# Kernel tuning notes

Measured on AMD Instinct MI355X. Metric: run time of the kernel, lower is better.

Reference implementation:

```python
import jax, jax.numpy as jnp
import numpy as np

C = 256
NUM_HEADS = 8
HEAD_DIM = C // NUM_HEADS
SCALE = HEAD_DIM ** -0.5


def setup_inputs() -> dict:
    key = jax.random.key(0)
    ks = jax.random.split(key, 10)
    B, H, W = 2, 64, 64
    s = 0.02
    return {
        "spatial_feat": jax.random.normal(ks[0], (B, C, H, W), jnp.float32),
        "freq_feat": jax.random.normal(ks[1], (B, C, H, W), jnp.float32),
        "wq": jax.random.normal(ks[2], (C, C), jnp.float32) * s,
        "bq": jax.random.normal(ks[3], (C,), jnp.float32) * s,
        "wk": jax.random.normal(ks[4], (C, C), jnp.float32) * s,
        "bk": jax.random.normal(ks[5], (C,), jnp.float32) * s,
        "wv": jax.random.normal(ks[6], (C, C), jnp.float32) * s,
        "bv": jax.random.normal(ks[7], (C,), jnp.float32) * s,
        "wo": jax.random.normal(ks[8], (C, C), jnp.float32) * s,
        "bo": jax.random.normal(ks[9], (C,), jnp.float32) * s,
    }


def _proj(x, w, b):
    # 1x1 conv == channel-mixing matmul: (O,C) x (B,C,H,W) -> (B,O,H,W)
    return jnp.einsum('oc,bchw->bohw', w, x) + b[None, :, None, None]


def _heads(x, B, HW):
    return x.reshape(B, NUM_HEADS, HEAD_DIM, HW)


def _cross_attend(q_src, kv_src, wq, bq, wk, bk, wv, bv, wo, bo):
    B, Cc, H, W = q_src.shape
    HW = H * W
    q = _heads(_proj(q_src, wq, bq), B, HW)   # (B, h, d, N)
    k = _heads(_proj(kv_src, wk, bk), B, HW)
    v = _heads(_proj(kv_src, wv, bv), B, HW)
    # attn[b,h,m,n] = q[...,m] . k[...,n]
    attn = jnp.einsum('bhdm,bhdn->bhmn', q, k) * SCALE
    attn = jax.nn.softmax(attn, axis=-1)
    # out[...,m] = sum_n v[...,n] * attn[m,n]
    out = jnp.einsum('bhdn,bhmn->bhdm', v, attn)
    out = out.reshape(B, Cc, H, W)
    return _proj(out, wo, bo)


def reference(spatial_feat, freq_feat, wq, bq, wk, bk, wv, bv, wo, bo):
    spatial_attended = spatial_feat + _cross_attend(
        spatial_feat, freq_feat, wq, bq, wk, bk, wv, bv, wo, bo)
    freq_attended = freq_feat + _cross_attend(
        freq_feat, spatial_feat, wq, bq, wk, bk, wv, bv, wo, bo)
    return spatial_attended + freq_attended
```

## Files before the change

kernel.cpp:

```cpp
#include <hip/hip_runtime.h>
#include <hip/hip_bf16.h>

#define B_ 2
#define C_ 256
#define NH_ 8
#define D_ 32
#define N_ 4096
#define SCALE_ 0.17677669529663689f
#define QSC_ 0.25505277f

typedef __hip_bfloat16 bf16;
typedef __attribute__((ext_vector_type(8))) short sx8;
typedef __attribute__((ext_vector_type(4))) short sx4;
typedef __attribute__((ext_vector_type(4))) float fx4;
typedef __attribute__((ext_vector_type(4))) int ix4;

__device__ __forceinline__ float b2f(bf16 x) { return __bfloat162float(x); }
__device__ __forceinline__ bf16 f2b(float x) { return __float2bfloat16(x); }
__device__ __forceinline__ short fbs(float x) { bf16 h = __float2bfloat16(x); return *(short*)&h; }
__device__ __forceinline__ float sbf(short s) { bf16 h = *(bf16*)&s; return __bfloat162float(h); }

#if __has_builtin(__builtin_amdgcn_exp2f)
__device__ __forceinline__ float fexp2(float x) { return __builtin_amdgcn_exp2f(x); }
#else
__device__ __forceinline__ float fexp2(float x) { return exp2f(x); }
#endif

__device__ __forceinline__ unsigned pkbf_tr(float x, float y) {
#if __has_builtin(__builtin_amdgcn_perm)
  return __builtin_amdgcn_perm(__builtin_bit_cast(unsigned, y),
                               __builtin_bit_cast(unsigned, x), 0x07060302u);
#else
  unsigned a = __builtin_bit_cast(unsigned, x) >> 16;
  unsigned b = __builtin_bit_cast(unsigned, y) & 0xFFFF0000u;
  return a | b;
#endif
}
__device__ __forceinline__ void pl32swap(unsigned &a, unsigned &b) {
  asm volatile("v_permlane32_swap_b32 %0, %1" : "+v"(a), "+v"(b));
}
__device__ __forceinline__ void pl16swap(unsigned &a, unsigned &b) {
  asm volatile("v_permlane16_swap_b32 %0, %1" : "+v"(a), "+v"(b));
}

__global__ __launch_bounds__(256)
void convert_kernel(const float* __restrict__ spatial,
                    const float* __restrict__ freq,
                    const float* __restrict__ wq, const float* __restrict__ wk,
                    const float* __restrict__ wv, const float* __restrict__ wo,
                    bf16* __restrict__ xb, bf16* __restrict__ wb,
                    bf16* __restrict__ wob) {
  const int tid = threadIdx.x;
  if (blockIdx.z == 4) {
    int base = (blockIdx.y * 64 + blockIdx.x) * 256 + tid;
    #pragma unroll
    for (int i = 0; i < 4; ++i) {
      int idx = base + i * 65536;
      if (idx < 196608) {
        const float* src = (idx < 65536) ? wq : (idx < 131072) ? wk : wv;
        wb[idx] = f2b(src[idx & 65535]);
      } else {
        wob[idx - 196608] = f2b(wo[idx - 196608]);
      }
    }
    return;
  }

  const int p0 = blockIdx.x * 64;
  const int c0 = blockIdx.y * 64;
  const int z  = blockIdx.z;
  const int s = z >> 1, b = z & 1;
  const float* x = (s == 0) ? spatial : freq;

  __shared__ float ls[64][65];

  const int pp = tid & 63, cb = tid >> 6;
  #pragma unroll
  for (int i = 0; i < 16; ++i) {
    int c = cb + 4 * i;
    ls[c][pp] = x[(size_t)(b * C_ + c0 + c) * N_ + p0 + pp];
  }
  __syncthreads();

  #pragma unroll
  for (int i = 0; i < 2; ++i) {
    int j = tid + 256 * i;
    int p = j >> 3, ck = (j & 7) * 8;
    short tmp[8];
    #pragma unroll
    for (int u = 0; u < 8; ++u) tmp[u] = fbs(ls[ck + u][p]);
    *(sx8*)(xb + ((size_t)z * N_ + p0 + p) * C_ + c0 + ck) = *(sx8*)tmp;
  }
}

__global__ __launch_bounds__(256)
void qkv_gemm_kernel(const bf16* __restrict__ wb, const bf16* __restrict__ xb,
                     const float* __restrict__ bq, const float* __restrict__ bk,
                     const float* __restrict__ bv,
                     bf16* __restrict__ qhf, bf16* __restrict__ khf,
                     bf16* __restrict__ vhf) {
  const int tid = threadIdx.x;
  const int p0 = blockIdx.x * 128;
  const int o0 = blockIdx.y * 128;
  const int z  = blockIdx.z;

  const int lane = tid & 63, w = tid >> 6;
  const int ml = lane & 15, Q4 = (lane >> 4) * 4, Q8 = (lane >> 4) * 8;
  const int ow = (w >> 1) * 64, pw = (w & 1) * 64;

  __shared__ __align__(16) short asb[128 * 72];
  __shared__ __align__(16) short bsb[128 * 72];
  __shared__ float bias_s[128];

  if (tid < 128) {
    int o = o0 + tid;
    bias_s[tid] = (o < 256) ? bq[o] : (o < 512) ? bk[o - 256] : bv[o - 512];
  }

  const fx4 z4 = {0.f, 0.f, 0.f, 0.f};
  fx4 acc[4][4];
  #pragma unroll
  for (int ot = 0; ot < 4; ++ot)
    #pragma unroll
    for (int pt = 0; pt < 4; ++pt) acc[ot][pt] = z4;

  const int sr = tid >> 1, scu = (tid & 1) * 32;
  for (int k0 = 0; k0 < 256; k0 += 64) {
    __syncthreads();
    #pragma unroll
    for (int u = 0; u < 4; ++u) {
      *(sx8*)&asb[sr * 72 + scu + u * 8] =
          *(const sx8*)&wb[(o0 + sr) * 256 + k0 + scu + u * 8];
      *(sx8*)&bsb[sr * 72 + scu + u * 8] =
          *(const sx8*)(xb + ((size_t)z * N_ + p0 + sr) * C_ + k0 + scu + u * 8);
    }
    __syncthreads();
    #pragma unroll
    for (int kk = 0; kk < 2; ++kk) {
      sx8 af[4], bfr[4];
      #pragma unroll
      for (int t = 0; t < 4; ++t)
        af[t] = *(sx8*)&asb[(ow + t * 16 + ml) * 72 + kk * 32 + Q8];
      #pragma unroll
      for (int t = 0; t < 4; ++t)
        bfr[t] = *(sx8*)&bsb[(pw + t * 16 + ml) * 72 + kk * 32 + Q8];
      #pragma unroll
      for (int ot = 0; ot < 4; ++ot)
        #pragma unroll
        for (int pt = 0; pt < 4; ++pt)
          acc[ot][pt] = __builtin_amdgcn_mfma_f32_16x16x32_bf16(
              af[ot], bfr[pt], acc[ot][pt], 0, 0, 0);
    }
  }

  if (o0 < 512) {
    bf16* dst = (o0 < 256) ? qhf : khf;
    const int ob = (o0 < 256) ? o0 : o0 - 256;
    const float scl = (o0 < 256) ? QSC_ : 1.f;
    #pragma unroll
    for (int ot = 0; ot < 4; ++ot) {
      const int og = ob + ow + ot * 16 + Q4;
      #pragma unroll
      for (int pt = 0; pt < 4; ++pt) {
        int p = p0 + pw + pt * 16 + ml;
        short tmp[4];
        #pragma unroll
        for (int r = 0; r < 4; ++r)
          tmp[r] = fbs((acc[ot][pt][r] + bias_s[ow + ot * 16 + Q4 + r]) * scl);
        *(sx4*)(dst + (((size_t)z * NH_ + (og >> 5)) * N_ + p) * D_ + (og & 31)) =
            *(sx4*)tmp;
      }
    }
  } else {
    #pragma unroll
    for (int ot = 0; ot < 4; ++ot)
      #pragma unroll
      for (int pt = 0; pt < 4; ++pt) {
        int p = p0 + pw + pt * 16 + ml;
        #pragma unroll
        for (int r = 0; r < 4; ++r) {
          int lo = ow + ot * 16 + Q4 + r;
          int rho = (o0 - 512) + lo;
          int h = rho >> 5, d = rho & 31;
          size_t basev = ((size_t)z * NH_ + h) * D_ * N_;
          vhf[basev + (size_t)(((p >> 5) * 2) + (d >> 4)) * 512 +
              (d & 15) * 32 + (p & 31)] = f2b(acc[ot][pt][r] + bias_s[lo]);
        }
      }
  }
}

__device__ __forceinline__ void attn_tile(const sx8 kf[4], const sx8 vf[2][2],
                                          const sx8 qf[4], sx8 onesf,
                                          fx4 acc[4][2], fx4 lacc[4]) {
  const fx4 z4 = {0.f, 0.f, 0.f, 0.f};
  #pragma unroll
  for (int s4 = 0; s4 < 4; ++s4) {
    fx4 st[4];
    __builtin_amdgcn_s_setprio(1);
    #pragma unroll
    for (int t = 0; t < 4; ++t)
      st[t] = __builtin_amdgcn_mfma_f32_16x16x32_bf16(kf[t], qf[s4], z4, 0, 0, 0);
    __builtin_amdgcn_s_setprio(0);

    unsigned T[4][2];
    #pragma unroll
    for (int t = 0; t < 4; ++t) {
      float e0 = fexp2(st[t][0]), e1 = fexp2(st[t][1]);
      float e2 = fexp2(st[t][2]), e3 = fexp2(st[t][3]);
      T[t][0] = pkbf_tr(e0, e1);
      T[t][1] = pkbf_tr(e2, e3);
    }
    pl32swap(T[0][0], T[1][0]); pl16swap(T[0][0], T[1][0]);
    pl32swap(T[0][1], T[1][1]); pl16swap(T[0][1], T[1][1]);
    pl32swap(T[2][0], T[3][0]); pl16swap(T[2][0], T[3][0]);
    pl32swap(T[2][1], T[3][1]); pl16swap(T[2][1], T[3][1]);
    ix4 p0 = {(int)T[0][0], (int)T[0][1], (int)T[1][0], (int)T[1][1]};
    ix4 p1 = {(int)T[2][0], (int)T[2][1], (int)T[3][0], (int)T[3][1]};
    sx8 pf0 = *(sx8*)&p0;
    sx8 pf1 = *(sx8*)&p1;

    __builtin_amdgcn_s_setprio(1);
    lacc[s4] = __builtin_amdgcn_mfma_f32_16x16x32_bf16(onesf, pf0, lacc[s4], 0, 0, 0);
    lacc[s4] = __builtin_amdgcn_mfma_f32_16x16x32_bf16(onesf, pf1, lacc[s4], 0, 0, 0);
    #pragma unroll
    for (int dt = 0; dt < 2; ++dt) {
      fx4 a = acc[s4][dt];
      a = __builtin_amdgcn_mfma_f32_16x16x32_bf16(vf[dt][0], pf0, a, 0, 0, 0);
      a = __builtin_amdgcn_mfma_f32_16x16x32_bf16(vf[dt][1], pf1, a, 0, 0, 0);
      acc[s4][dt] = a;
    }
    __builtin_amdgcn_s_setprio(0);
  }
}

__global__ __launch_bounds__(256, 2)
void attn_kernel(const bf16* __restrict__ qhf, const bf16* __restrict__ khf,
                 const bf16* __restrict__ vhf, bf16* __restrict__ attoT) {
  const int tid  = threadIdx.x;
  const int m0   = blockIdx.x * 256;
  const int h    = blockIdx.y;
  const int z    = blockIdx.z;
  const int s = z >> 1, b = z & 1;
  const int zo = ((1 - s) << 1) | b;

  const bf16* qz = qhf + ((size_t)z  * NH_ + h) * N_ * D_;
  const bf16* kz = khf + ((size_t)zo * NH_ + h) * N_ * D_;
  const bf16* vz = vhf + ((size_t)zo * NH_ + h) * D_ * N_;

  const int lane = tid & 63;
  const int w    = tid >> 6;
  const int ml   = lane & 15;
  const int q4   = lane >> 4;
  const int Q4   = q4 * 4;
  const int Q8   = q4 * 8;

  sx8 qf[4];
  #pragma unroll
  for (int s4 = 0; s4 < 4; ++s4)
    qf[s4] = *(const sx8*)(qz + (size_t)(m0 + w * 64 + s4 * 16 + ml) * D_ + Q8);

  sx8 onesf;
  #pragma unroll
  for (int u = 0; u < 8; ++u) onesf[u] = (short)0x3F80;

  const fx4 z4 = {0.f, 0.f, 0.f, 0.f};
  fx4 acc[4][2];
  #pragma unroll
  for (int s4 = 0; s4 < 4; ++s4) { acc[s4][0] = z4; acc[s4][1] = z4; }
  fx4 lacc[4] = {z4, z4, z4, z4};

  const bf16* kbase = kz + (size_t)ml * D_ + Q8;
  const bf16* vbase = vz + (size_t)ml * 32 + Q8;

#define LDK(n0, kf)                                                          \
  {                                                                          \
    _Pragma("unroll") for (int t = 0; t < 4; ++t)                            \
        kf[t] = *(const sx8*)(kbase + (size_t)((n0) + t * 16) * D_);         \
  }
#define LDV(n0, vf)                                                          \
  {                                                                          \
    _Pragma("unroll") for (int dt = 0; dt < 2; ++dt)                         \
        _Pragma("unroll") for (int c = 0; c < 2; ++c)                        \
            vf[dt][c] = *(const sx8*)(vbase +                                \
                (size_t)(((n0) >> 5) + c) * 1024 + dt * 512);                \
  }

  sx8 kfA[4], kfB[4], vfA[2][2], vfB[2][2];
  LDK(0, kfA);
  LDV(0, vfA);

  #pragma unroll 1
  for (int n0 = 0; n0 < N_; n0 += 128) {
    const int nn = n0 + 64;
    LDK(nn, kfB);
    LDV(nn, vfB);
    attn_tile(kfA, vfA, qf, onesf, acc, lacc);

    const int nn2 = (nn + 64 < N_) ? nn + 64 : 0;
    LDK(nn2, kfA);
    LDV(nn2, vfA);
    attn_tile(kfB, vfB, qf, onesf, acc, lacc);
  }
#undef LDK
#undef LDV

  #pragma unroll
  for (int s4 = 0; s4 < 4; ++s4) {
    float inv = 1.f / lacc[s4][0];
    int col = m0 + w * 64 + s4 * 16 + ml;
    #pragma unroll
    for (int dt = 0; dt < 2; ++dt) {
      short tmp[4];
      #pragma unroll
      for (int r = 0; r < 4; ++r) tmp[r] = fbs(acc[s4][dt][r] * inv);
      *(sx4*)(attoT + ((size_t)z * N_ + col) * C_ + h * D_ + dt * 16 + Q4) =
          *(sx4*)tmp;
    }
  }
}

__global__ __launch_bounds__(256)
void out_proj_kernel(const bf16* __restrict__ wob, const bf16* __restrict__ attoT,
                     const float* __restrict__ spatial,
                     const float* __restrict__ freq,
                     const float* __restrict__ bo, float* __restrict__ out) {
  const int tid = threadIdx.x;
  const int p0 = blockIdx.x * 64;
  const int o0 = blockIdx.y * 64;
  const int b  = blockIdx.z;

  const int lane = tid & 63, w = tid >> 6;
  const int ml = lane & 15, Q4 = (lane >> 4) * 4, Q8 = (lane >> 4) * 8;
  const int ow = (w >> 1) * 32, pw = (w & 1) * 32;

  __shared__ __align__(16) short asb[64 * 72];
  __shared__ __align__(16) short bsb[64 * 72];
  __shared__ float bo_s[64];

  if (tid < 64) bo_s[tid] = 2.f * bo[o0 + tid];

  const bf16* at0 = attoT + (size_t)(0 + b) * N_ * C_;
  const bf16* at1 = attoT + (size_t)(2 + b) * N_ * C_;

  const fx4 z4 = {0.f, 0.f, 0.f, 0.f};
  fx4 acc[2][2];
  #pragma unroll
  for (int ot = 0; ot < 2; ++ot)
    #pragma unroll
    for (int pt = 0; pt < 2; ++pt) acc[ot][pt] = z4;

  for (int k0 = 0; k0 < 256; k0 += 64) {
    __syncthreads();
    #pragma unroll
    for (int i = 0; i < 2; ++i) {
      int j = tid + 256 * i;
      int r = j >> 3, cu = (j & 7) * 8;
      *(sx8*)&asb[r * 72 + cu] = *(const sx8*)&wob[(o0 + r) * 256 + k0 + cu];
      sx8 va = *(const sx8*)(at0 + (size_t)(p0 + r) * C_ + k0 + cu);
      sx8 vb2 = *(const sx8*)(at1 + (size_t)(p0 + r) * C_ + k0 + cu);
      short tmp[8];
      #pragma unroll
      for (int u = 0; u < 8; ++u) tmp[u] = fbs(sbf(va[u]) + sbf(vb2[u]));
      *(sx8*)&bsb[r * 72 + cu] = *(sx8*)tmp;
    }
    __syncthreads();
    #pragma unroll
    for (int kk = 0; kk < 2; ++kk) {
      sx8 af[2], bfr[2];
      #pragma unroll
      for (int t = 0; t < 2; ++t)
        af[t] = *(sx8*)&asb[(ow + t * 16 + ml) * 72 + kk * 32 + Q8];
      #pragma unroll
      for (int t = 0; t < 2; ++t)
        bfr[t] = *(sx8*)&bsb[(pw + t * 16 + ml) * 72 + kk * 32 + Q8];
      #pragma unroll
      for (int ot = 0; ot < 2; ++ot)
        #pragma unroll
        for (int pt = 0; pt < 2; ++pt)
          acc[ot][pt] = __builtin_amdgcn_mfma_f32_16x16x32_bf16(
              af[ot], bfr[pt], acc[ot][pt], 0, 0, 0);
    }
  }

  #pragma unroll
  for (int ot = 0; ot < 2; ++ot)
    #pragma unroll
    for (int pt = 0; pt < 2; ++pt) {
      int p = p0 + pw + pt * 16 + ml;
      #pragma unroll
      for (int r = 0; r < 4; ++r) {
        int ol = ow + ot * 16 + Q4 + r;
        size_t off = ((size_t)b * C_ + o0 + ol) * N_ + p;
        out[off] = acc[ot][pt][r] + bo_s[ol] + spatial[off] + freq[off];
      }
    }
}

extern "C" void kernel_launch(void* const* d_in, const int* in_sizes, int n_in,
                              void* d_out, int out_size, void* d_ws, size_t ws_size,
                              hipStream_t stream) {
  const float* spatial = (const float*)d_in[0];
  const float* freq    = (const float*)d_in[1];
  const float* wq = (const float*)d_in[2];
  const float* bq = (const float*)d_in[3];
  const float* wk = (const float*)d_in[4];
  const float* bk = (const float*)d_in[5];
  const float* wv = (const float*)d_in[6];
  const float* bv = (const float*)d_in[7];
  const float* wo = (const float*)d_in[8];
  const float* bo = (const float*)d_in[9];
  float* out = (float*)d_out;

  const size_t SZ = (size_t)2 * B_ * N_ * C_;
  bf16* xb    = (bf16*)d_ws;
  bf16* qhf   = xb + SZ;
  bf16* khf   = qhf + SZ;
  bf16* vhf   = khf + SZ;
  bf16* attoT = vhf + SZ;
  bf16* wb    = attoT + SZ;
  bf16* wob   = wb + 768 * 256;

  convert_kernel<<<dim3(N_ / 64, C_ / 64, 5), 256, 0, stream>>>(
      spatial, freq, wq, wk, wv, wo, xb, wb, wob);
  qkv_gemm_kernel<<<dim3(N_ / 128, 768 / 128, 2 * B_), 256, 0, stream>>>(
      wb, xb, bq, bk, bv, qhf, khf, vhf);
  attn_kernel<<<dim3(N_ / 256, NH_, 2 * B_), 256, 0, stream>>>(
      qhf, khf, vhf, attoT);
  out_proj_kernel<<<dim3(N_ / 64, C_ / 64, B_), 256, 0, stream>>>(
      wob, attoT, spatial, freq, bo, out);
}
```

Before: 195.1 us.

## Split attention key range into two halves and combine in output projection

The attention kernel now splits the key/value sequence into two halves handled by separate blocks, doubling the grid. Each block writes unnormalized partial outputs and its row sums. The output-projection kernel loads both partials, sums them and divides by the combined sums while staging its operand tile. The aim is more concurrent work and higher occupancy (launch bounds raised to 4 blocks per CU). The cost is extra partial-output traffic, a larger workspace, and a possible register limit that may cause spills in the attention loop.

```diff
diff --git a/kernel.cpp b/kernel.cpp
--- a/kernel.cpp
+++ b/kernel.cpp
@@ -6,6 +6,7 @@
 #define NH_ 8
 #define D_ 32
 #define N_ 4096
+#define NHALF_ 2048
 #define SCALE_ 0.17677669529663689f
 #define QSC_ 0.25505277f
 
@@ -234,19 +235,23 @@
   }
 }
 
-__global__ __launch_bounds__(256, 2)
+__global__ __launch_bounds__(256, 4)
 void attn_kernel(const bf16* __restrict__ qhf, const bf16* __restrict__ khf,
-                 const bf16* __restrict__ vhf, bf16* __restrict__ attoT) {
+                 const bf16* __restrict__ vhf, bf16* __restrict__ attoT,
+                 float* __restrict__ lws) {
   const int tid  = threadIdx.x;
   const int m0   = blockIdx.x * 256;
   const int h    = blockIdx.y;
-  const int z    = blockIdx.z;
+  const int zz   = blockIdx.z;
+  const int z    = zz >> 1, half = zz & 1;
   const int s = z >> 1, b = z & 1;
   const int zo = ((1 - s) << 1) | b;
 
   const bf16* qz = qhf + ((size_t)z  * NH_ + h) * N_ * D_;
-  const bf16* kz = khf + ((size_t)zo * NH_ + h) * N_ * D_;
-  const bf16* vz = vhf + ((size_t)zo * NH_ + h) * D_ * N_;
+  const bf16* kz = khf + ((size_t)zo * NH_ + h) * N_ * D_ +
+                   (size_t)half * NHALF_ * D_;
+  const bf16* vz = vhf + ((size_t)zo * NH_ + h) * D_ * N_ +
+                   (size_t)half * (NHALF_ / 32) * 1024;
 
   const int lane = tid & 63;
   const int w    = tid >> 6;
@@ -291,13 +296,13 @@
   LDV(0, vfA);
 
   #pragma unroll 1
-  for (int n0 = 0; n0 < N_; n0 += 128) {
+  for (int n0 = 0; n0 < NHALF_; n0 += 128) {
     const int nn = n0 + 64;
     LDK(nn, kfB);
     LDV(nn, vfB);
     attn_tile(kfA, vfA, qf, onesf, acc, lacc);
 
-    const int nn2 = (nn + 64 < N_) ? nn + 64 : 0;
+    const int nn2 = (nn + 64 < NHALF_) ? nn + 64 : 0;
     LDK(nn2, kfA);
     LDV(nn2, vfA);
     attn_tile(kfB, vfB, qf, onesf, acc, lacc);
@@ -305,16 +310,18 @@
 #undef LDK
 #undef LDV
 
+  bf16* ath = attoT + (size_t)half * (2 * B_ * N_ * C_);
   #pragma unroll
   for (int s4 = 0; s4 < 4; ++s4) {
-    float inv = 1.f / lacc[s4][0];
     int col = m0 + w * 64 + s4 * 16 + ml;
+    if (q4 == 0)
+      lws[(((size_t)half * 2 * B_ + z) * NH_ + h) * N_ + col] = lacc[s4][0];
     #pragma unroll
     for (int dt = 0; dt < 2; ++dt) {
       short tmp[4];
       #pragma unroll
-      for (int r = 0; r < 4; ++r) tmp[r] = fbs(acc[s4][dt][r] * inv);
-      *(sx4*)(attoT + ((size_t)z * N_ + col) * C_ + h * D_ + dt * 16 + Q4) =
+      for (int r = 0; r < 4; ++r) tmp[r] = fbs(acc[s4][dt][r]);
+      *(sx4*)(ath + ((size_t)z * N_ + col) * C_ + h * D_ + dt * 16 + Q4) =
           *(sx4*)tmp;
     }
   }
@@ -322,6 +329,7 @@
 
 __global__ __launch_bounds__(256)
 void out_proj_kernel(const bf16* __restrict__ wob, const bf16* __restrict__ attoT,
+                     const float* __restrict__ lws,
                      const float* __restrict__ spatial,
                      const float* __restrict__ freq,
                      const float* __restrict__ bo, float* __restrict__ out) {
@@ -337,11 +345,22 @@
   __shared__ __align__(16) short asb[64 * 72];
   __shared__ __align__(16) short bsb[64 * 72];
   __shared__ float bo_s[64];
+  __shared__ float linv[2][NH_][64];
 
   if (tid < 64) bo_s[tid] = 2.f * bo[o0 + tid];
-
-  const bf16* at0 = attoT + (size_t)(0 + b) * N_ * C_;
-  const bf16* at1 = attoT + (size_t)(2 + b) * N_ * C_;
+  const size_t HSZ = (size_t)2 * B_ * N_ * C_;
+  for (int i = tid; i < 2 * NH_ * 64; i += 256) {
+    int si = i >> 9, hi = (i >> 6) & (NH_ - 1), pi = i & 63;
+    int zl = si * 2 + b;
+    float l0 = lws[(((size_t)0 * 2 * B_ + zl) * NH_ + hi) * N_ + p0 + pi];
+    float l1 = lws[(((size_t)1 * 2 * B_ + zl) * NH_ + hi) * N_ + p0 + pi];
+    linv[si][hi][pi] = 1.f / (l0 + l1);
+  }
+
+  const bf16* a0s = attoT + (size_t)(0 + b) * N_ * C_;
+  const bf16* a0f = attoT + (size_t)(2 + b) * N_ * C_;
+  const bf16* a1s = attoT + HSZ + (size_t)(0 + b) * N_ * C_;
+  const bf16* a1f = attoT + HSZ + (size_t)(2 + b) * N_ * C_;
 
   const fx4 z4 = {0.f, 0.f, 0.f, 0.f};
   fx4 acc[2][2];
@@ -357,11 +376,19 @@
       int j = tid + 256 * i;
       int r = j >> 3, cu = (j & 7) * 8;
       *(sx8*)&asb[r * 72 + cu] = *(const sx8*)&wob[(o0 + r) * 256 + k0 + cu];
-      sx8 va = *(const sx8*)(at0 + (size_t)(p0 + r) * C_ + k0 + cu);
-      sx8 vb2 = *(const sx8*)(at1 + (size_t)(p0 + r) * C_ + k0 + cu);
+      size_t aoff = (size_t)(p0 + r) * C_ + k0 + cu;
+      sx8 v0s = *(const sx8*)(a0s + aoff);
+      sx8 v1s = *(const sx8*)(a1s + aoff);
+      sx8 v0f = *(const sx8*)(a0f + aoff);
+      sx8 v1f = *(const sx8*)(a1f + aoff);
+      int hidx = (k0 + cu) >> 5;
+      float is = linv[0][hidx][r];
+      float ifr = linv[1][hidx][r];
       short tmp[8];
       #pragma unroll
-      for (int u = 0; u < 8; ++u) tmp[u] = fbs(sbf(va[u]) + sbf(vb2[u]));
+      for (int u = 0; u < 8; ++u)
+        tmp[u] = fbs((sbf(v0s[u]) + sbf(v1s[u])) * is +
+                     (sbf(v0f[u]) + sbf(v1f[u])) * ifr);
       *(sx8*)&bsb[r * 72 + cu] = *(sx8*)tmp;
     }
     __syncthreads();
@@ -418,15 +445,16 @@
   bf16* khf   = qhf + SZ;
   bf16* vhf   = khf + SZ;
   bf16* attoT = vhf + SZ;
-  bf16* wb    = attoT + SZ;
+  bf16* wb    = attoT + 2 * SZ;
   bf16* wob   = wb + 768 * 256;
+  float* lws  = (float*)(wob + 256 * 256);
 
   convert_kernel<<<dim3(N_ / 64, C_ / 64, 5), 256, 0, stream>>>(
       spatial, freq, wq, wk, wv, wo, xb, wb, wob);
   qkv_gemm_kernel<<<dim3(N_ / 128, 768 / 128, 2 * B_), 256, 0, stream>>>(
       wb, xb, bq, bk, bv, qhf, khf, vhf);
-  attn_kernel<<<dim3(N_ / 256, NH_, 2 * B_), 256, 0, stream>>>(
-      qhf, khf, vhf, attoT);
+  attn_kernel<<<dim3(N_ / 256, NH_, 2 * B_ * 2), 256, 0, stream>>>(
+      qhf, khf, vhf, attoT, lws);
   out_proj_kernel<<<dim3(N_ / 64, C_ / 64, B_), 256, 0, stream>>>(
-      wob, attoT, spatial, freq, bo, out);
-}
+      wob, attoT, lws, spatial, freq, bo, out);
+}
```

Result: slower. 477.4 us (+144.6%).
